# Performance work log

Hardware: AMD Instinct MI355X
Metric: run time of the kernel (lower is better)

The kernel has to match this reference:

```python
import jax, jax.numpy as jnp
import numpy as np
from jax import lax

B, C, H, L = 4, 64, 8, 2048  # batch, per-head channels, heads, sequence length


def setup_inputs() -> dict:
    key = jax.random.key(0)
    ks = jax.random.split(key, 15)

    def p(k, shape, s=0.05):
        return jax.random.normal(k, shape, jnp.float32) * s

    inp = {"x": jax.random.normal(ks[0], (B, C, L), jnp.float32)}
    for i, nm in enumerate(["q", "k", "v"]):
        inp[f"{nm}_dw"] = p(ks[1 + 4 * i], (C, 1, 3))       # depthwise conv weight, groups=C, k=3
        inp[f"{nm}_db"] = p(ks[2 + 4 * i], (C,))
        inp[f"{nm}_pw"] = p(ks[3 + 4 * i], (H * C, C))      # pointwise 1x1 conv weight
        inp[f"{nm}_pb"] = p(ks[4 + 4 * i], (H * C,))
    inp["u_w"] = p(ks[13], (C, H * C))                      # unify_heads 1x1 conv weight
    inp["u_b"] = p(ks[14], (C,))
    return inp


def dsconv(x, dw, db, pw, pb):
    # Depth-separable conv1d: depthwise (k=3, pad=1, groups=C) then pointwise 1x1.
    c = x.shape[1]
    y = lax.conv_general_dilated(x, dw, window_strides=(1,), padding=[(1, 1)],
                                 dimension_numbers=("NCH", "OIH", "NCH"),
                                 feature_group_count=c)
    y = y + db[None, :, None]
    return jnp.einsum("bcl,oc->bol", y, pw) + pb[None, :, None]


def reference(x, q_dw, q_db, q_pw, q_pb, k_dw, k_db, k_pw, k_pb,
              v_dw, v_db, v_pw, v_pb, u_w, u_b):
    b, c, l = x.shape
    h = H
    scale = c ** (-0.25)
    q = dsconv(x, q_dw, q_db, q_pw, q_pb).reshape(b, h, c, l) * scale
    k = dsconv(x, k_dw, k_db, k_pw, k_pb).reshape(b, h, c, l) * scale
    v = dsconv(x, v_dw, v_db, v_pw, v_pb).reshape(b, h, c, l)
    # dot[b,h,i,j] = sum_c k[b,h,c,i] * q[b,h,c,j]  (i = key pos, j = query pos)
    dot = jnp.einsum("bhci,bhcj->bhij", k, q)
    att = jax.nn.softmax(dot, axis=2)  # normalize over key positions (torch dim=1 of [bh,l,l])
    out = jnp.einsum("bhci,bhij->bhcj", v, att).reshape(b, h * c, l)
    return jnp.einsum("bkl,ck->bcl", out, u_w) + u_b[None, :, None]
```

## Files before the change

### kernel.cpp

```cpp
#include <hip/hip_runtime.h>
#include <hip/hip_bf16.h>
#include <stdint.h>
#include <string.h>

typedef unsigned short u16;
typedef unsigned int u32;
typedef __bf16 bf16x8 __attribute__((ext_vector_type(8)));
typedef float f32x4 __attribute__((ext_vector_type(4)));

#define NB 4
#define NC 64
#define NH 8
#define NL 2048
#define HC 512

#define XT_OFF  ((size_t)0)
#define WM_OFF  ((size_t)1 << 20)
#define PBM_OFF ((size_t)2 << 20)
#define V_OFF   ((size_t)4 << 20)
#define QT_OFF  ((size_t)12 << 20)
#define KT_OFF  ((size_t)20 << 20)

#define LP 68

#if __has_builtin(__builtin_amdgcn_exp2f)
#define EXP2F __builtin_amdgcn_exp2f
#else
#define EXP2F exp2f
#endif

static __device__ __forceinline__ u16 f2bfu(float f) {
  union { float f; unsigned int i; } x; x.f = f;
  unsigned int i = x.i;
  return (u16)((i + 0x7fffu + ((i >> 16) & 1u)) >> 16);
}
static __device__ __forceinline__ u32 pk2(float a, float b) {
  float2 f; f.x = a; f.y = b;
  __hip_bfloat162 h = __float22bfloat162_rn(f);
  u32 w; __builtin_memcpy(&w, &h, 4); return w;
}
static __device__ __forceinline__ bf16x8 ld_bf8(const u16* p) {
  bf16x8 v; __builtin_memcpy(&v, p, 16); return v;
}

__global__ __launch_bounds__(256) void prep_all(
    const float* __restrict__ x,
    const float* __restrict__ qdw, const float* __restrict__ qdb,
    const float* __restrict__ qpw, const float* __restrict__ qpb,
    const float* __restrict__ kdw, const float* __restrict__ kdb,
    const float* __restrict__ kpw, const float* __restrict__ kpb,
    const float* __restrict__ vdw, const float* __restrict__ vdb,
    const float* __restrict__ vpw, const float* __restrict__ vpb,
    const float* __restrict__ ub,
    u16* __restrict__ Wm, float* __restrict__ pbm,
    u16* __restrict__ xT, float* __restrict__ out)
{
  __shared__ __align__(16) u16 T[64 * LP];
  int bx = blockIdx.x;
  int tid = threadIdx.x;

  if (bx < 512) {
    int i4 = bx * 256 + tid;
    int c = (i4 >> 9) & 63;
    float f = ub[c];
    float4 v = {f, f, f, f};
    ((float4*)out)[i4] = v;
    return;
  }
  if (bx < 902) {
    int idx = (bx - 512) * 256 + tid;
    if (idx < 98304) {
      int tns = idx >> 15, r = idx & 32767, o = r >> 6, c = r & 63;
      const float* dw = (tns == 0) ? qdw : (tns == 1) ? kdw : vdw;
      const float* pw = (tns == 0) ? qpw : (tns == 1) ? kpw : vpw;
      float s = (tns == 0) ? 0.35355339059327373f * 1.4426950408889634f
              : (tns == 1) ? 0.35355339059327373f : 1.0f;
      float w = pw[o * 64 + c] * s;
#pragma unroll
      for (int d = 0; d < 3; ++d)
        Wm[((size_t)(tns * 3 + d) * 512 + o) * 64 + c] = f2bfu(w * dw[c * 3 + d]);
    } else {
      int i = idx - 98304;
      int tns = i >> 9, o = i & 511;
      const float* db = (tns == 0) ? qdb : (tns == 1) ? kdb : vdb;
      const float* pw = (tns == 0) ? qpw : (tns == 1) ? kpw : vpw;
      const float* pb = (tns == 0) ? qpb : (tns == 1) ? kpb : vpb;
      float s = (tns == 0) ? 0.35355339059327373f * 1.4426950408889634f
              : (tns == 1) ? 0.35355339059327373f : 1.0f;
      float bias = pb[o];
      for (int c = 0; c < 64; ++c) bias += pw[o * 64 + c] * db[c];
      pbm[i] = bias * s;
    }
    return;
  }
  {
    int b2 = bx - 902;
    int lt = b2 & 31, b = b2 >> 5;
    {
      int c = tid & 63, ls = (tid >> 6) * 16;
      const float4* g = (const float4*)(x + ((size_t)b * NC + c) * NL + lt * 64 + ls);
      u16 tmp[16];
#pragma unroll
      for (int j4 = 0; j4 < 4; ++j4) {
        float4 f = g[j4];
        tmp[j4*4+0] = f2bfu(f.x); tmp[j4*4+1] = f2bfu(f.y);
        tmp[j4*4+2] = f2bfu(f.z); tmp[j4*4+3] = f2bfu(f.w);
      }
#pragma unroll
      for (int j = 0; j < 16; ++j) T[(ls + j) * LP + c] = tmp[j];
    }
    __syncthreads();
    {
      int r = tid >> 2, cs = (tid & 3) * 16;
      uint4 a = *(const uint4*)&T[r * LP + cs];
      uint4 b3 = *(const uint4*)&T[r * LP + cs + 8];
      u16* o = xT + ((size_t)b * NL + lt * 64 + r) * 64 + cs;
      *(uint4*)o = a;
      *(uint4*)(o + 8) = b3;
    }
  }
}

__global__ __launch_bounds__(256) void qkv_gemm(
    const u16* __restrict__ xT, const u16* __restrict__ Wm,
    const float* __restrict__ pbm,
    u16* __restrict__ v, u16* __restrict__ qT, u16* __restrict__ kT)
{
  __shared__ __align__(16) u16 WS[3][64 * LP];
  __shared__ __align__(16) u16 XS[2][66 * LP];
  __shared__ __align__(16) u16 OS[64 * LP];

  int bx = blockIdx.x;
  int lg  = bx & 7;
  int och = (bx >> 3) & 7;
  int tmp = bx >> 6;
  int tns = tmp % 3;
  int b   = tmp / 3;

  int tid = threadIdx.x;
  int wave = tid >> 6, lane = tid & 63, quad = lane >> 4, l16 = lane & 15;
  const u16* xg = xT + (size_t)b * NL * 64;

  {
    const u16* wg = Wm + ((size_t)(tns * 3) * 512 + och * 64) * 64;
#pragma unroll
    for (int it = 0; it < 6; ++it) {
      int s = tid + it * 256;
      int d = s >> 9, r = s & 511;
      int o = r >> 3, c4 = r & 7;
      uint4 w = *(const uint4*)(wg + ((size_t)d * 512 + o) * 64 + c4 * 8);
      *(uint4*)&WS[d][o * LP + c4 * 8] = w;
    }
  }

  int xr0 = tid >> 3,          xc0 = (tid & 7) * 8;
  int xr1 = (tid + 256) >> 3,  xc1 = xc0;
  int xr2 = (tid + 512) >> 3,  xc2 = xc0;
  uint4 R0, R1, R2;
  uint4 Z = {0, 0, 0, 0};

#define LOAD_XS(tt)                                                         \
  {                                                                         \
    int base = (lg * 4 + (tt)) * 64 - 1;                                    \
    int g0 = base + xr0, g1 = base + xr1, g2 = base + xr2;                  \
    R0 = ((unsigned)g0 < NL) ? *(const uint4*)(xg + (size_t)g0 * 64 + xc0) : Z; \
    R1 = ((unsigned)g1 < NL) ? *(const uint4*)(xg + (size_t)g1 * 64 + xc1) : Z; \
    if (tid < 16)                                                           \
      R2 = ((unsigned)g2 < NL) ? *(const uint4*)(xg + (size_t)g2 * 64 + xc2) : Z; \
  }
#define STORE_XS(bf)                                                        \
  {                                                                         \
    *(uint4*)&XS[bf][xr0 * LP + xc0] = R0;                                  \
    *(uint4*)&XS[bf][xr1 * LP + xc1] = R1;                                  \
    if (tid < 16) *(uint4*)&XS[bf][xr2 * LP + xc2] = R2;                    \
  }

  LOAD_XS(0); STORE_XS(0);
  LOAD_XS(1);
  __syncthreads();

  float bias4[4];
  bf16x8 aw[3][2];
  if (tns == 2) {
    const float* pbt = pbm + tns * 512 + och * 64 + wave * 16;
#pragma unroll
    for (int rr = 0; rr < 4; ++rr) bias4[rr] = pbt[quad * 4 + rr];
#pragma unroll
    for (int d = 0; d < 3; ++d)
#pragma unroll
      for (int kh = 0; kh < 2; ++kh)
        aw[d][kh] = ld_bf8(&WS[d][(wave * 16 + l16) * LP + kh * 32 + quad * 8]);
  } else {
    const float* pbt = pbm + tns * 512 + och * 64;
#pragma unroll
    for (int nt = 0; nt < 4; ++nt) bias4[nt] = pbt[nt * 16 + l16];
  }

  for (int t = 0; t < 4; ++t) {
    int cur = t & 1;
    f32x4 acc[4] = {{0,0,0,0},{0,0,0,0},{0,0,0,0},{0,0,0,0}};

    if (tns == 2) {
#pragma unroll
      for (int nt = 0; nt < 4; ++nt)
#pragma unroll
        for (int d = 0; d < 3; ++d)
#pragma unroll
          for (int kh = 0; kh < 2; ++kh) {
            bf16x8 bx8 = ld_bf8(&XS[cur][(nt * 16 + l16 + d) * LP + kh * 32 + quad * 8]);
            acc[nt] = __builtin_amdgcn_mfma_f32_16x16x32_bf16(aw[d][kh], bx8, acc[nt], 0, 0, 0);
          }
    } else {
      bf16x8 ax[3][2];
#pragma unroll
      for (int d = 0; d < 3; ++d)
#pragma unroll
        for (int kh = 0; kh < 2; ++kh)
          ax[d][kh] = ld_bf8(&XS[cur][(wave * 16 + l16 + d) * LP + kh * 32 + quad * 8]);
#pragma unroll
      for (int nt = 0; nt < 4; ++nt)
#pragma unroll
        for (int d = 0; d < 3; ++d)
#pragma unroll
          for (int kh = 0; kh < 2; ++kh) {
            bf16x8 bw = ld_bf8(&WS[d][(nt * 16 + l16) * LP + kh * 32 + quad * 8]);
            acc[nt] = __builtin_amdgcn_mfma_f32_16x16x32_bf16(ax[d][kh], bw, acc[nt], 0, 0, 0);
          }
    }

    if (t < 3) { STORE_XS((t + 1) & 1); if (t < 2) LOAD_XS(t + 2); }
    __syncthreads();

    if (tns == 2) {
#pragma unroll
      for (int nt = 0; nt < 4; ++nt)
#pragma unroll
        for (int rr = 0; rr < 4; ++rr)
          OS[(wave * 16 + quad * 4 + rr) * LP + nt * 16 + l16] =
              f2bfu(acc[nt][rr] + bias4[rr]);
    } else {
#pragma unroll
      for (int nt = 0; nt < 4; ++nt)
#pragma unroll
        for (int rr = 0; rr < 4; ++rr)
          OS[(wave * 16 + quad * 4 + rr) * LP + nt * 16 + l16] =
              f2bfu(acc[nt][rr] + bias4[nt]);
    }
    __syncthreads();

    {
      int lt = lg * 4 + t;
      int r = tid >> 2, ck = (tid & 3) * 16;
      uint4 a = *(const uint4*)&OS[r * LP + ck];
      uint4 b2 = *(const uint4*)&OS[r * LP + ck + 8];
      u16* gp;
      if (tns == 2)
        gp = v + ((size_t)(b * HC + och * 64 + r)) * NL + lt * 64 + ck;
      else {
        u16* dst = (tns == 0) ? qT : kT;
        gp = dst + ((size_t)(b * 8 + och) * NL + lt * 64 + r) * 64 + ck;
      }
      *(uint4*)gp = a;
      *(uint4*)(gp + 8) = b2;
    }
  }
#undef LOAD_XS
#undef STORE_XS
}

__global__ __launch_bounds__(256) void attn_kernel(
    const u16* __restrict__ qT, const u16* __restrict__ kT,
    const u16* __restrict__ vg, const float* __restrict__ uw,
    float* __restrict__ outg)
{
  __shared__ __align__(16) u16 Kt[2][64 * LP];
  __shared__ __align__(16) u16 Vt[2][64 * LP];
  __shared__ __align__(16) u16 UW[64 * LP];
  __shared__ __align__(16) u16 QP[128 * LP];

  int bx = blockIdx.x;
  int qt = bx & 15, bh = bx >> 4;
  int b = bh >> 3, h = bh & 7;
  int tid = threadIdx.x;
  int wave = tid >> 6, lane = tid & 63, quad = lane >> 4, l16 = lane & 15;

  const u16* Qh = qT + (size_t)bh * NL * 64;
  const u16* Kh = kT + (size_t)bh * NL * 64;
  const u16* Vh = vg + ((size_t)(b * HC + h * NC)) * NL;
  int q0 = qt * 128;

  int sr = tid >> 2, ss = (tid & 3) * 16;
  int vc = tid & 63, vk = (tid >> 6) * 16;

  {
    int r = tid >> 1, cs = (tid & 1) * 32;
    const u16* g = Qh + (size_t)(q0 + r) * 64 + cs;
    uint4 a0 = *(const uint4*)g;
    uint4 a1 = *(const uint4*)(g + 8);
    uint4 a2 = *(const uint4*)(g + 16);
    uint4 a3 = *(const uint4*)(g + 24);
    u16* d = &QP[r * LP + cs];
    *(uint4*)d = a0; *(uint4*)(d + 8) = a1;
    *(uint4*)(d + 16) = a2; *(uint4*)(d + 24) = a3;
  }
  {
    int c = tid >> 2, g = (tid & 3) * 16;
    const float4* s = (const float4*)(uw + (size_t)c * HC + h * 64 + g);
#pragma unroll
    for (int j = 0; j < 4; ++j) {
      float4 w = s[j];
      u16* d = &UW[c * LP + g + j * 4];
      d[0] = f2bfu(w.x); d[1] = f2bfu(w.y); d[2] = f2bfu(w.z); d[3] = f2bfu(w.w);
    }
  }

  uint4 ka, kb, va, vb;
  {
    const u16* ks = Kh + (size_t)sr * 64 + ss;
    ka = *(const uint4*)ks; kb = *(const uint4*)(ks + 8);
    const u16* vs = Vh + (size_t)vc * NL + vk;
    va = *(const uint4*)vs; vb = *(const uint4*)(vs + 8);
    *(uint4*)&Kt[0][sr * LP + ss] = ka;
    *(uint4*)&Kt[0][sr * LP + ss + 8] = kb;
    *(uint4*)&Vt[0][vc * LP + vk] = va;
    *(uint4*)&Vt[0][vc * LP + vk + 8] = vb;
    const u16* ks1 = Kh + (size_t)(64 + sr) * 64 + ss;
    ka = *(const uint4*)ks1; kb = *(const uint4*)(ks1 + 8);
    const u16* vs1 = Vh + (size_t)vc * NL + 64 + vk;
    va = *(const uint4*)vs1; vb = *(const uint4*)(vs1 + 8);
  }
  __syncthreads();

  bf16x8 bq[2][2];
#pragma unroll
  for (int t = 0; t < 2; ++t)
#pragma unroll
    for (int kh = 0; kh < 2; ++kh)
      bq[t][kh] = ld_bf8(&QP[(wave * 32 + t * 16 + l16) * LP + kh * 32 + quad * 8]);

  f32x4 o[2][4];
#pragma unroll
  for (int t = 0; t < 2; ++t)
#pragma unroll
    for (int ct = 0; ct < 4; ++ct) o[t][ct] = (f32x4){0, 0, 0, 0};
  float l_part[2] = {0.f, 0.f};

  u16* Pw = &QP[wave * 32 * LP];

  for (int i = 0; i < 32; ++i) {
    int cur = i & 1;
    bf16x8 ak[4][2], av[4][2];
#pragma unroll
    for (int j = 0; j < 4; ++j)
#pragma unroll
      for (int kh = 0; kh < 2; ++kh) {
        ak[j][kh] = ld_bf8(&Kt[cur][(j * 16 + l16) * LP + kh * 32 + quad * 8]);
        av[j][kh] = ld_bf8(&Vt[cur][(j * 16 + l16) * LP + kh * 32 + quad * 8]);
      }

#pragma unroll
    for (int t = 0; t < 2; ++t) {
      f32x4 s[4];
#pragma unroll
      for (int ktl = 0; ktl < 4; ++ktl) {
        f32x4 z = {0, 0, 0, 0};
        z = __builtin_amdgcn_mfma_f32_16x16x32_bf16(ak[ktl][0], bq[t][0], z, 0, 0, 0);
        z = __builtin_amdgcn_mfma_f32_16x16x32_bf16(ak[ktl][1], bq[t][1], z, 0, 0, 0);
        s[ktl] = z;
      }
      u16* Pq = &Pw[(t * 16 + l16) * LP];
#pragma unroll
      for (int ktl = 0; ktl < 4; ++ktl) {
        float p0 = EXP2F(s[ktl][0]);
        float p1 = EXP2F(s[ktl][1]);
        float p2 = EXP2F(s[ktl][2]);
        float p3 = EXP2F(s[ktl][3]);
        l_part[t] += p0 + p1 + p2 + p3;
        *(u32*)&Pq[ktl * 16 + quad * 4] = pk2(p0, p1);
        *(u32*)&Pq[ktl * 16 + quad * 4 + 2] = pk2(p2, p3);
      }
#pragma unroll
      for (int kh = 0; kh < 2; ++kh) {
        bf16x8 bp = ld_bf8(&Pq[kh * 32 + quad * 8]);
#pragma unroll
        for (int ct = 0; ct < 4; ++ct)
          o[t][ct] = __builtin_amdgcn_mfma_f32_16x16x32_bf16(av[ct][kh], bp, o[t][ct], 0, 0, 0);
      }
    }

    if (i < 31) {
      int nxt = cur ^ 1;
      *(uint4*)&Kt[nxt][sr * LP + ss] = ka;
      *(uint4*)&Kt[nxt][sr * LP + ss + 8] = kb;
      *(uint4*)&Vt[nxt][vc * LP + vk] = va;
      *(uint4*)&Vt[nxt][vc * LP + vk + 8] = vb;
      if (i < 30) {
        int kt2 = (i + 2) * 64;
        const u16* ks = Kh + (size_t)(kt2 + sr) * 64 + ss;
        ka = *(const uint4*)ks; kb = *(const uint4*)(ks + 8);
        const u16* vs = Vh + (size_t)vc * NL + kt2 + vk;
        va = *(const uint4*)vs; vb = *(const uint4*)(vs + 8);
      }
    }
    __syncthreads();
  }

  float* ob = outg + ((size_t)b * NC) * NL;
#pragma unroll
  for (int t = 0; t < 2; ++t) {
    float lp = l_part[t];
    lp += __shfl_xor(lp, 16);
    lp += __shfl_xor(lp, 32);
    float rinv = 1.0f / lp;
    u16* OT = &Pw[(t * 16 + l16) * LP];
    *(u32*)&OT[ 0 + quad * 4]     = pk2(o[t][0][0]*rinv, o[t][0][1]*rinv);
    *(u32*)&OT[ 0 + quad * 4 + 2] = pk2(o[t][0][2]*rinv, o[t][0][3]*rinv);
    *(u32*)&OT[16 + quad * 4]     = pk2(o[t][1][0]*rinv, o[t][1][1]*rinv);
    *(u32*)&OT[16 + quad * 4 + 2] = pk2(o[t][1][2]*rinv, o[t][1][3]*rinv);
    *(u32*)&OT[32 + quad * 4]     = pk2(o[t][2][0]*rinv, o[t][2][1]*rinv);
    *(u32*)&OT[32 + quad * 4 + 2] = pk2(o[t][2][2]*rinv, o[t][2][3]*rinv);
    *(u32*)&OT[48 + quad * 4]     = pk2(o[t][3][0]*rinv, o[t][3][1]*rinv);
    *(u32*)&OT[48 + quad * 4 + 2] = pk2(o[t][3][2]*rinv, o[t][3][3]*rinv);

    int qcol = q0 + wave * 32 + t * 16 + l16;
#pragma unroll
    for (int mt = 0; mt < 4; ++mt) {
      f32x4 acc = {0, 0, 0, 0};
#pragma unroll
      for (int kh = 0; kh < 2; ++kh) {
        bf16x8 a = ld_bf8(&UW[(mt * 16 + l16) * LP + kh * 32 + quad * 8]);
        bf16x8 bt = ld_bf8(&OT[kh * 32 + quad * 8]);
        acc = __builtin_amdgcn_mfma_f32_16x16x32_bf16(a, bt, acc, 0, 0, 0);
      }
#pragma unroll
      for (int rr = 0; rr < 4; ++rr) {
        int c = mt * 16 + quad * 4 + rr;
        atomicAdd(&ob[(size_t)c * NL + qcol], acc[rr]);
      }
    }
  }
}

extern "C" void kernel_launch(void* const* d_in, const int* in_sizes, int n_in,
                              void* d_out, int out_size, void* d_ws, size_t ws_size,
                              hipStream_t stream) {
  (void)in_sizes; (void)n_in; (void)out_size; (void)ws_size;
  const float* x   = (const float*)d_in[0];
  const float* qdw = (const float*)d_in[1];
  const float* qdb = (const float*)d_in[2];
  const float* qpw = (const float*)d_in[3];
  const float* qpb = (const float*)d_in[4];
  const float* kdw = (const float*)d_in[5];
  const float* kdb = (const float*)d_in[6];
  const float* kpw = (const float*)d_in[7];
  const float* kpb = (const float*)d_in[8];
  const float* vdw = (const float*)d_in[9];
  const float* vdb = (const float*)d_in[10];
  const float* vpw = (const float*)d_in[11];
  const float* vpb = (const float*)d_in[12];
  const float* uw  = (const float*)d_in[13];
  const float* ub  = (const float*)d_in[14];

  char* ws = (char*)d_ws;
  u16*   xT  = (u16*)(ws + XT_OFF);
  u16*   Wm  = (u16*)(ws + WM_OFF);
  float* pbm = (float*)(ws + PBM_OFF);
  u16*   v   = (u16*)(ws + V_OFF);
  u16*   qT  = (u16*)(ws + QT_OFF);
  u16*   kT  = (u16*)(ws + KT_OFF);
  float* out = (float*)d_out;

  prep_all<<<1030, 256, 0, stream>>>(
      x, qdw, qdb, qpw, qpb, kdw, kdb, kpw, kpb, vdw, vdb, vpw, vpb,
      ub, Wm, pbm, xT, out);
  qkv_gemm<<<768, 256, 0, stream>>>(xT, Wm, pbm, v, qT, kT);
  attn_kernel<<<512, 256, 0, stream>>>(qT, kT, v, uw, out);
}
```

Before: 157.7 us.

## Relayout P and O fragments in registers via permlane swaps instead of LDS

Replaces the LDS round trip used to convert the softmax P tile (and the normalized output tile) from MFMA accumulator layout to B-operand layout with permlane32/permlane16 swap instructions that run entirely in registers. Q fragments are now loaded straight from global memory, so the QP shared buffer is gone and shared memory use drops, which may allow higher occupancy. It also adds s_setprio hints around the MFMA bursts to favour matrix issue across waves. The cost is extra cross-lane permute instructions, and the kernel now needs the gfx950 permlane swap builtins.

Result: slower. 167.2 us (+6.0%).

```diff
diff --git a/kernel.cpp b/kernel.cpp
--- a/kernel.cpp
+++ b/kernel.cpp
@@ -7,6 +7,7 @@
 typedef unsigned int u32;
 typedef __bf16 bf16x8 __attribute__((ext_vector_type(8)));
 typedef float f32x4 __attribute__((ext_vector_type(4)));
+typedef unsigned int u32x2v __attribute__((ext_vector_type(2)));
 
 #define NB 4
 #define NC 64
@@ -42,6 +43,17 @@
 static __device__ __forceinline__ bf16x8 ld_bf8(const u16* p) {
   bf16x8 v; __builtin_memcpy(&v, p, 16); return v;
 }
+static __device__ __forceinline__ bf16x8 frag_from4(u32 a, u32 b, u32 c, u32 d) {
+  u32 t[4] = {a, b, c, d};
+  bf16x8 v; __builtin_memcpy(&v, t, 16); return v;
+}
+
+#define XCHG(X_, Y_, Fa_, Fb_)                                              \
+  {                                                                         \
+    u32x2v a_ = __builtin_amdgcn_permlane32_swap((X_), (Y_), false, false); \
+    u32x2v b_ = __builtin_amdgcn_permlane16_swap(a_.x, a_.y, false, false); \
+    Fa_ = b_.x; Fb_ = b_.y;                                                 \
+  }
 
 __global__ __launch_bounds__(256) void prep_all(
     const float* __restrict__ x,
@@ -276,7 +288,6 @@
   __shared__ __align__(16) u16 Kt[2][64 * LP];
   __shared__ __align__(16) u16 Vt[2][64 * LP];
   __shared__ __align__(16) u16 UW[64 * LP];
-  __shared__ __align__(16) u16 QP[128 * LP];
 
   int bx = blockIdx.x;
   int qt = bx & 15, bh = bx >> 4;
@@ -292,17 +303,6 @@
   int sr = tid >> 2, ss = (tid & 3) * 16;
   int vc = tid & 63, vk = (tid >> 6) * 16;
 
-  {
-    int r = tid >> 1, cs = (tid & 1) * 32;
-    const u16* g = Qh + (size_t)(q0 + r) * 64 + cs;
-    uint4 a0 = *(const uint4*)g;
-    uint4 a1 = *(const uint4*)(g + 8);
-    uint4 a2 = *(const uint4*)(g + 16);
-    uint4 a3 = *(const uint4*)(g + 24);
-    u16* d = &QP[r * LP + cs];
-    *(uint4*)d = a0; *(uint4*)(d + 8) = a1;
-    *(uint4*)(d + 16) = a2; *(uint4*)(d + 24) = a3;
-  }
   {
     int c = tid >> 2, g = (tid & 3) * 16;
     const float4* s = (const float4*)(uw + (size_t)c * HC + h * 64 + g);
@@ -329,14 +329,16 @@
     const u16* vs1 = Vh + (size_t)vc * NL + 64 + vk;
     va = *(const uint4*)vs1; vb = *(const uint4*)(vs1 + 8);
   }
+
+  bf16x8 bq[2][2];
+#pragma unroll
+  for (int t = 0; t < 2; ++t)
+#pragma unroll
+    for (int kh = 0; kh < 2; ++kh)
+      bq[t][kh] = ld_bf8(Qh + (size_t)(q0 + wave * 32 + t * 16 + l16) * 64 +
+                         kh * 32 + quad * 8);
+
   __syncthreads();
-
-  bf16x8 bq[2][2];
-#pragma unroll
-  for (int t = 0; t < 2; ++t)
-#pragma unroll
-    for (int kh = 0; kh < 2; ++kh)
-      bq[t][kh] = ld_bf8(&QP[(wave * 32 + t * 16 + l16) * LP + kh * 32 + quad * 8]);
 
   f32x4 o[2][4];
 #pragma unroll
@@ -344,8 +346,6 @@
 #pragma unroll
     for (int ct = 0; ct < 4; ++ct) o[t][ct] = (f32x4){0, 0, 0, 0};
   float l_part[2] = {0.f, 0.f};
-
-  u16* Pw = &QP[wave * 32 * LP];
 
   for (int i = 0; i < 32; ++i) {
     int cur = i & 1;
@@ -361,6 +361,7 @@
 #pragma unroll
     for (int t = 0; t < 2; ++t) {
       f32x4 s[4];
+      __builtin_amdgcn_s_setprio(1);
 #pragma unroll
       for (int ktl = 0; ktl < 4; ++ktl) {
         f32x4 z = {0, 0, 0, 0};
@@ -368,23 +369,29 @@
         z = __builtin_amdgcn_mfma_f32_16x16x32_bf16(ak[ktl][1], bq[t][1], z, 0, 0, 0);
         s[ktl] = z;
       }
-      u16* Pq = &Pw[(t * 16 + l16) * LP];
+      __builtin_amdgcn_s_setprio(0);
+      u32 w01[4], w23[4];
 #pragma unroll
       for (int ktl = 0; ktl < 4; ++ktl) {
         float p0 = EXP2F(s[ktl][0]);
         float p1 = EXP2F(s[ktl][1]);
         float p2 = EXP2F(s[ktl][2]);
         float p3 = EXP2F(s[ktl][3]);
-        l_part[t] += p0 + p1 + p2 + p3;
-        *(u32*)&Pq[ktl * 16 + quad * 4] = pk2(p0, p1);
-        *(u32*)&Pq[ktl * 16 + quad * 4 + 2] = pk2(p2, p3);
+        l_part[t] += (p0 + p1) + (p2 + p3);
+        w01[ktl] = pk2(p0, p1);
+        w23[ktl] = pk2(p2, p3);
       }
 #pragma unroll
       for (int kh = 0; kh < 2; ++kh) {
-        bf16x8 bp = ld_bf8(&Pq[kh * 32 + quad * 8]);
+        u32 F0, F1, F2, F3;
+        XCHG(w01[2 * kh], w01[2 * kh + 1], F0, F2);
+        XCHG(w23[2 * kh], w23[2 * kh + 1], F1, F3);
+        bf16x8 bp = frag_from4(F0, F1, F2, F3);
+        __builtin_amdgcn_s_setprio(1);
 #pragma unroll
         for (int ct = 0; ct < 4; ++ct)
           o[t][ct] = __builtin_amdgcn_mfma_f32_16x16x32_bf16(av[ct][kh], bp, o[t][ct], 0, 0, 0);
+        __builtin_amdgcn_s_setprio(0);
       }
     }
 
@@ -412,15 +419,21 @@
     lp += __shfl_xor(lp, 16);
     lp += __shfl_xor(lp, 32);
     float rinv = 1.0f / lp;
-    u16* OT = &Pw[(t * 16 + l16) * LP];
-    *(u32*)&OT[ 0 + quad * 4]     = pk2(o[t][0][0]*rinv, o[t][0][1]*rinv);
-    *(u32*)&OT[ 0 + quad * 4 + 2] = pk2(o[t][0][2]*rinv, o[t][0][3]*rinv);
-    *(u32*)&OT[16 + quad * 4]     = pk2(o[t][1][0]*rinv, o[t][1][1]*rinv);
-    *(u32*)&OT[16 + quad * 4 + 2] = pk2(o[t][1][2]*rinv, o[t][1][3]*rinv);
-    *(u32*)&OT[32 + quad * 4]     = pk2(o[t][2][0]*rinv, o[t][2][1]*rinv);
-    *(u32*)&OT[32 + quad * 4 + 2] = pk2(o[t][2][2]*rinv, o[t][2][3]*rinv);
-    *(u32*)&OT[48 + quad * 4]     = pk2(o[t][3][0]*rinv, o[t][3][1]*rinv);
-    *(u32*)&OT[48 + quad * 4 + 2] = pk2(o[t][3][2]*rinv, o[t][3][3]*rinv);
+
+    u32 w01[4], w23[4];
+#pragma unroll
+    for (int ct = 0; ct < 4; ++ct) {
+      w01[ct] = pk2(o[t][ct][0] * rinv, o[t][ct][1] * rinv);
+      w23[ct] = pk2(o[t][ct][2] * rinv, o[t][ct][3] * rinv);
+    }
+    bf16x8 ot[2];
+#pragma unroll
+    for (int kh = 0; kh < 2; ++kh) {
+      u32 F0, F1, F2, F3;
+      XCHG(w01[2 * kh], w01[2 * kh + 1], F0, F2);
+      XCHG(w23[2 * kh], w23[2 * kh + 1], F1, F3);
+      ot[kh] = frag_from4(F0, F1, F2, F3);
+    }
 
     int qcol = q0 + wave * 32 + t * 16 + l16;
 #pragma unroll
@@ -429,8 +442,7 @@
 #pragma unroll
       for (int kh = 0; kh < 2; ++kh) {
         bf16x8 a = ld_bf8(&UW[(mt * 16 + l16) * LP + kh * 32 + quad * 8]);
-        bf16x8 bt = ld_bf8(&OT[kh * 32 + quad * 8]);
-        acc = __builtin_amdgcn_mfma_f32_16x16x32_bf16(a, bt, acc, 0, 0, 0);
+        acc = __builtin_amdgcn_mfma_f32_16x16x32_bf16(a, ot[kh], acc, 0, 0, 0);
       }
 #pragma unroll
       for (int rr = 0; rr < 4; ++rr) {
```
